# Kernel optimization log

Hardware: AMD Instinct MI355X
Metric: run time of the kernel (lower is better)

Reference implementation:

```python
import jax, jax.numpy as jnp
import numpy as np

B, S, D, H, FF = 2, 2048, 1024, 16, 4096
HD = D // H
SCALE = 1.0 / np.sqrt(HD).astype(np.float32)
EPS = 1e-5


def _ln(x, g, b):
    m = jnp.mean(x, axis=-1, keepdims=True)
    v = jnp.mean((x - m) ** 2, axis=-1, keepdims=True)
    return (x - m) * jax.lax.rsqrt(v + EPS) * g + b


def setup_inputs() -> dict:
    key = jax.random.key(0)
    ks = jax.random.split(key, 8)
    def lin(k, fan_in, shape):
        return (jax.random.normal(k, shape, jnp.float32) / np.sqrt(fan_in)).astype(jnp.float32)
    return {
        "x": jax.random.normal(ks[0], (B, S, D), jnp.float32),
        "w_qkv": lin(ks[1], D, (D, 3 * D)),          # qkv_proj (no bias)
        "w_o": lin(ks[2], D, (D, D)),                 # out_proj
        "b_o": jnp.zeros((D,), jnp.float32),
        "g1": jnp.ones((D,), jnp.float32),            # attn LayerNorm
        "bt1": jnp.zeros((D,), jnp.float32),
        "w1": lin(ks[3], D, (D, FF)),                 # FFN linear1
        "b1": jnp.zeros((FF,), jnp.float32),
        "w2": lin(ks[4], FF, (FF, D)),                # FFN linear2
        "b2": jnp.zeros((D,), jnp.float32),
        "g2": jnp.ones((D,), jnp.float32),            # FFN LayerNorm
        "bt2": jnp.zeros((D,), jnp.float32),
    }


def reference(x, w_qkv, w_o, b_o, g1, bt1, w1, b1, w2, b2, g2, bt2):
    # --- MultiHeadAttention (post-LN, dropout=eval/identity) ---
    qkv = (x @ w_qkv).reshape(B, S, H, 3 * HD)
    q, k, v = jnp.split(qkv, 3, axis=-1)  # each [B,S,H,HD]
    # kernel_func = scaled softmax over keys
    scores = jnp.einsum("bihd,bjhd->bhij", q, k) * SCALE  # [B,H,S,S]
    attn = jax.nn.softmax(scores, axis=-1)
    ao = jnp.einsum("bhij,bjhd->bihd", attn, v).reshape(B, S, D)
    y = _ln(x + ao @ w_o + b_o, g1, bt1)
    # --- FFN (post-LN) ---
    h = jax.nn.relu(y @ w1 + b1)
    return _ln(y + h @ w2 + b2, g2, bt2)
```

## Files before the change

kernel.cpp:

```cpp
#include <hip/hip_runtime.h>
#include <hip/hip_bf16.h>

#define B_  2
#define S_  2048
#define D_  1024
#define H_  16
#define HD_ 64
#define FF_ 4096
#define NT  (B_ * S_)
#define SCALE_ 0.125f
#define KLOG2E 0.1803368801111f
#define EPS_  1e-5f

typedef __attribute__((ext_vector_type(8))) short bf16x8;
typedef __attribute__((ext_vector_type(4))) float f32x4;

__device__ inline short f2bf(float f) {
    __hip_bfloat16 h = __float2bfloat16(f);
    return __builtin_bit_cast(short, h);
}
__device__ inline float bf2f(unsigned short u) {
    __hip_bfloat16 h = __builtin_bit_cast(__hip_bfloat16, u);
    return __bfloat162float(h);
}
__device__ inline unsigned int pk2bf(float lo, float hi) {
    __hip_bfloat162 h = __float22bfloat162_rn(float2{lo, hi});
    const unsigned short l16 = __builtin_bit_cast(unsigned short, h.x);
    const unsigned short h16 = __builtin_bit_cast(unsigned short, h.y);
    return (unsigned int)l16 | ((unsigned int)h16 << 16);
}

#define GLOBAL_AS __attribute__((address_space(1)))
#define LDS_AS    __attribute__((address_space(3)))

struct DetectArgs { const unsigned short* p[12]; int n[12]; };

__global__ __launch_bounds__(256) void detect_kernel(DetectArgs a, int* flags) {
    const int t = blockIdx.x;
    const unsigned short* s = a.p[t];
    const int cnt = min(a.n[t], 16384);
    const int tid = threadIdx.x;
    int huge = 0, zeven = 0;
    for (int i = tid; i < cnt; i += 256) {
        const unsigned short v = s[i];
        const int e = (v >> 7) & 0xFF;
        if (e >= 142) huge++;
        if (((i & 1) == 0) && ((v & 0x7FFF) == 0)) zeven++;
    }
    __shared__ int sh, sz;
    if (tid == 0) { sh = 0; sz = 0; }
    __syncthreads();
    atomicAdd(&sh, huge);
    atomicAdd(&sz, zeven);
    __syncthreads();
    if (tid == 0) flags[t] = (sh > 0 || sz * 4 > cnt) ? 1 : 0;
}

struct VecArgs { const void* src[7]; float* dst[7]; int n[7]; int fidx[7]; };

__global__ __launch_bounds__(256) void conv_x_vecs_kernel(
    const void* __restrict__ src, unsigned short* __restrict__ dst, int n,
    VecArgs a, const int* __restrict__ flags)
{
    const int i = blockIdx.x * 256 + threadIdx.x;
    if (i < n) {
        if (flags[0])
            dst[i] = (unsigned short)f2bf(((const float*)src)[i]);
        else
            dst[i] = ((const unsigned short*)src)[i];
    }
    if (blockIdx.x < 7) {
        const int v = blockIdx.x;
        const int f = flags[a.fidx[v]];
        for (int j = threadIdx.x; j < a.n[v]; j += 256) {
            a.dst[v][j] = f ? ((const float*)a.src[v])[j]
                            : bf2f(((const unsigned short*)a.src[v])[j]);
        }
    }
}

struct TArgs {
    const void* src[4]; unsigned short* dst[4];
    int K[4], N[4], fidx[4], start[5];
};

__global__ __launch_bounds__(256) void conv_t_all_kernel(
    TArgs t, const int* __restrict__ flags)
{
    __shared__ short T[32][33];
    const int tile = blockIdx.x;
    int w = 0;
    if (tile >= t.start[1]) w = 1;
    if (tile >= t.start[2]) w = 2;
    if (tile >= t.start[3]) w = 3;
    const int rel = tile - t.start[w];
    const int K = t.K[w], N = t.N[w];
    const int tilesN = N / 32;
    const int kt = (rel / tilesN) * 32, nt = (rel % tilesN) * 32;
    const void* src = t.src[w];
    unsigned short* dst = t.dst[w];
    const int f = flags[t.fidx[w]];

    const int c  = threadIdx.x & 31;
    const int r0 = (threadIdx.x >> 5) * 4;
#pragma unroll
    for (int i = 0; i < 4; i++) {
        const int r = r0 + i;
        const size_t gi = (size_t)(kt + r) * N + nt + c;
        short v = f ? f2bf(((const float*)src)[gi])
                    : (short)((const unsigned short*)src)[gi];
        T[c][r] = v;
    }
    __syncthreads();
#pragma unroll
    for (int i = 0; i < 4; i++) {
        const int n = r0 + i;
        dst[(size_t)(nt + n) * K + kt + c] = (unsigned short)T[n][c];
    }
}

template<bool HAS_BIAS, bool RELU, int RES, bool OUT_F32, bool QSCALE>
__global__ __launch_bounds__(256) void gemm128_kernel(
    const unsigned short* __restrict__ A,
    const unsigned short* __restrict__ Bt,
    const float* __restrict__ bias,
    const unsigned short* __restrict__ resb,
    const float* __restrict__ resf,
    const int* __restrict__ flags,
    void* __restrict__ out,
    int M, int N, int K)
{
    __shared__ short As[2][128 * 32];
    __shared__ short Bs[2][128 * 32];

    const int tid  = threadIdx.x;
    const int wave = tid >> 6;
    const int lane = tid & 63;
    const int quad = lane >> 4;
    const int l16  = lane & 15;

    const int row0 = blockIdx.x * 128;
    const int col0 = blockIdx.y * 128;

    const int ldrow = lane >> 2;
    const int ldk   = (lane & 3) * 8;
    const unsigned short* agp0 = A  + (size_t)(row0 + wave * 32 + ldrow) * K + ldk;
    const unsigned short* agp1 = agp0 + (size_t)16 * K;
    const unsigned short* bgp0 = Bt + (size_t)(col0 + wave * 32 + ldrow) * K + ldk;
    const unsigned short* bgp1 = bgp0 + (size_t)16 * K;

    const int wm = (wave >> 1) * 64;
    const int wn = (wave & 1) * 64;

    f32x4 acc[4][4] = {};

    for (int k0 = 0; k0 < K; k0 += 64) {
#pragma unroll
        for (int h = 0; h < 2; h++) {
            __builtin_amdgcn_global_load_lds(
                (const GLOBAL_AS void*)(agp0 + k0 + h * 32),
                (LDS_AS void*)&As[h][wave * 1024 + lane * 8], 16, 0, 0);
            __builtin_amdgcn_global_load_lds(
                (const GLOBAL_AS void*)(agp1 + k0 + h * 32),
                (LDS_AS void*)&As[h][wave * 1024 + 512 + lane * 8], 16, 0, 0);
            __builtin_amdgcn_global_load_lds(
                (const GLOBAL_AS void*)(bgp0 + k0 + h * 32),
                (LDS_AS void*)&Bs[h][wave * 1024 + lane * 8], 16, 0, 0);
            __builtin_amdgcn_global_load_lds(
                (const GLOBAL_AS void*)(bgp1 + k0 + h * 32),
                (LDS_AS void*)&Bs[h][wave * 1024 + 512 + lane * 8], 16, 0, 0);
        }
        __syncthreads();

#pragma unroll
        for (int h = 0; h < 2; h++) {
            bf16x8 af[4], bfr[4];
#pragma unroll
            for (int mi = 0; mi < 4; mi++)
                af[mi] = *reinterpret_cast<const bf16x8*>(
                    &As[h][(wm + mi * 16 + l16) * 32 + quad * 8]);
#pragma unroll
            for (int ni = 0; ni < 4; ni++)
                bfr[ni] = *reinterpret_cast<const bf16x8*>(
                    &Bs[h][(wn + ni * 16 + l16) * 32 + quad * 8]);
#pragma unroll
            for (int mi = 0; mi < 4; mi++)
#pragma unroll
                for (int ni = 0; ni < 4; ni++)
                    acc[mi][ni] = __builtin_amdgcn_mfma_f32_16x16x32_bf16(
                        af[mi], bfr[ni], acc[mi][ni], 0, 0, 0);
        }
        __syncthreads();
    }

    int resIsF32 = 0;
    if constexpr (RES == 2) resIsF32 = flags[0];

#pragma unroll
    for (int ni = 0; ni < 4; ni++) {
        const int col = col0 + wn + ni * 16 + l16;
        float badd = 0.f;
        if constexpr (HAS_BIAS) badd = bias[col];
        float qs = 1.f;
        if constexpr (QSCALE)
            qs = (((col0 + wn + ni * 16) % 192) < 64) ? KLOG2E : 1.f;
#pragma unroll
        for (int mi = 0; mi < 4; mi++) {
#pragma unroll
            for (int r = 0; r < 4; r++) {
                const int row = row0 + wm + mi * 16 + quad * 4 + r;
                float v = acc[mi][ni][r] + badd;
                if constexpr (QSCALE) v *= qs;
                if constexpr (RES == 1) {
                    v += bf2f(resb[(size_t)row * N + col]);
                } else if constexpr (RES == 2) {
                    v += resIsF32 ? resf[(size_t)row * N + col]
                                  : bf2f(resb[(size_t)row * N + col]);
                }
                if constexpr (RELU) v = fmaxf(v, 0.f);
                if constexpr (OUT_F32)
                    ((float*)out)[(size_t)row * N + col] = v;
                else
                    ((unsigned short*)out)[(size_t)row * N + col] =
                        (unsigned short)f2bf(v);
            }
        }
    }
}

__global__ __launch_bounds__(256) void gemm128_sk_kernel(
    const unsigned short* __restrict__ A,
    const unsigned short* __restrict__ Bt,
    float* __restrict__ out0,
    float* __restrict__ out1,
    int M, int N, int K)
{
    __shared__ short As[2][128 * 32];
    __shared__ short Bs[2][128 * 32];

    const int tid  = threadIdx.x;
    const int wave = tid >> 6;
    const int lane = tid & 63;
    const int quad = lane >> 4;
    const int l16  = lane & 15;

    const int row0 = blockIdx.x * 128;
    const int col0 = blockIdx.y * 128;
    const int z    = blockIdx.z;
    const int Kh   = K >> 1;

    const unsigned short* Az  = A  + (size_t)z * Kh;
    const unsigned short* Btz = Bt + (size_t)z * Kh;
    float* out = z ? out1 : out0;

    const int ldrow = lane >> 2;
    const int ldk   = (lane & 3) * 8;
    const unsigned short* agp0 = Az  + (size_t)(row0 + wave * 32 + ldrow) * K + ldk;
    const unsigned short* agp1 = agp0 + (size_t)16 * K;
    const unsigned short* bgp0 = Btz + (size_t)(col0 + wave * 32 + ldrow) * K + ldk;
    const unsigned short* bgp1 = bgp0 + (size_t)16 * K;

    const int wm = (wave >> 1) * 64;
    const int wn = (wave & 1) * 64;

    f32x4 acc[4][4] = {};

    for (int k0 = 0; k0 < Kh; k0 += 64) {
#pragma unroll
        for (int h = 0; h < 2; h++) {
            __builtin_amdgcn_global_load_lds(
                (const GLOBAL_AS void*)(agp0 + k0 + h * 32),
                (LDS_AS void*)&As[h][wave * 1024 + lane * 8], 16, 0, 0);
            __builtin_amdgcn_global_load_lds(
                (const GLOBAL_AS void*)(agp1 + k0 + h * 32),
                (LDS_AS void*)&As[h][wave * 1024 + 512 + lane * 8], 16, 0, 0);
            __builtin_amdgcn_global_load_lds(
                (const GLOBAL_AS void*)(bgp0 + k0 + h * 32),
                (LDS_AS void*)&Bs[h][wave * 1024 + lane * 8], 16, 0, 0);
            __builtin_amdgcn_global_load_lds(
                (const GLOBAL_AS void*)(bgp1 + k0 + h * 32),
                (LDS_AS void*)&Bs[h][wave * 1024 + 512 + lane * 8], 16, 0, 0);
        }
        __syncthreads();

#pragma unroll
        for (int h = 0; h < 2; h++) {
            bf16x8 af[4], bfr[4];
#pragma unroll
            for (int mi = 0; mi < 4; mi++)
                af[mi] = *reinterpret_cast<const bf16x8*>(
                    &As[h][(wm + mi * 16 + l16) * 32 + quad * 8]);
#pragma unroll
            for (int ni = 0; ni < 4; ni++)
                bfr[ni] = *reinterpret_cast<const bf16x8*>(
                    &Bs[h][(wn + ni * 16 + l16) * 32 + quad * 8]);
#pragma unroll
            for (int mi = 0; mi < 4; mi++)
#pragma unroll
                for (int ni = 0; ni < 4; ni++)
                    acc[mi][ni] = __builtin_amdgcn_mfma_f32_16x16x32_bf16(
                        af[mi], bfr[ni], acc[mi][ni], 0, 0, 0);
        }
        __syncthreads();
    }

#pragma unroll
    for (int ni = 0; ni < 4; ni++) {
        const int col = col0 + wn + ni * 16 + l16;
#pragma unroll
        for (int mi = 0; mi < 4; mi++)
#pragma unroll
            for (int r = 0; r < 4; r++) {
                const int row = row0 + wm + mi * 16 + quad * 4 + r;
                out[(size_t)row * N + col] = acc[mi][ni][r];
            }
    }
}

__global__ __launch_bounds__(512) void attn_kernel(
    const unsigned short* __restrict__ qkv,
    unsigned short* __restrict__ ao)
{
    extern __shared__ char smem[];

    const int qt = blockIdx.x;
    const int h  = blockIdx.y;
    const int b  = blockIdx.z;

    const int tid  = threadIdx.x;
    const int wave = tid >> 6;
    const int g    = wave >> 2;
    const int gw   = wave & 3;
    const int lane = tid & 63;
    const int quad = lane >> 4;
    const int l16  = lane & 15;
    const int gtid = tid & 255;

    short* Ks = (short*)smem + g * (64 * 72);
    short* Vt = (short*)(smem + 18432) + g * (64 * 72);
    short* Ps = (short*)(smem + 36864) + wave * (32 * 72);

    bf16x8 qf[2][2];
#pragma unroll
    for (int mi = 0; mi < 2; mi++) {
        const int qrow = qt * 128 + gw * 32 + mi * 16 + l16;
        const unsigned short* qb = qkv + (size_t)(b * S_ + qrow) * 3072 + h * 192;
        qf[mi][0] = *reinterpret_cast<const bf16x8*>(qb + quad * 8);
        qf[mi][1] = *reinterpret_cast<const bf16x8*>(qb + 32 + quad * 8);
    }

    bf16x8 vones;
#pragma unroll
    for (int j = 0; j < 8; j++) vones[j] = (short)0x3F80;

    f32x4 o[2][4] = {};
    f32x4 o_l[2] = {};

    const int skey = gtid >> 3;
    const int soct = gtid & 7;
    const int vp   = gtid >> 3;
    const int kA   = (vp & 15) + ((vp >> 4) << 5);
    const int kB   = kA + 16;
    const int posA = 4 * (vp & 15) + 2 * (vp >> 4);
    const int vwr  = ((posA >> 3) ^ soct) * 8 + (posA & 7);

    const int kb0   = g * (S_ / 2);
    const int kbend = kb0 + S_ / 2;

    const unsigned short* kbase0 = qkv + (size_t)(b * S_) * 3072 + h * 192 + 64;
    const unsigned short* vbase0 = qkv + (size_t)(b * S_) * 3072 + h * 192 + 128;

    bf16x8 pk0 = *reinterpret_cast<const bf16x8*>(kbase0 + (size_t)(kb0 + skey) * 3072 + soct * 8);
    bf16x8 pk1 = *reinterpret_cast<const bf16x8*>(kbase0 + (size_t)(kb0 + skey + 32) * 3072 + soct * 8);
    bf16x8 pv0 = *reinterpret_cast<const bf16x8*>(vbase0 + (size_t)(kb0 + kA) * 3072 + soct * 8);
    bf16x8 pv1 = *reinterpret_cast<const bf16x8*>(vbase0 + (size_t)(kb0 + kB) * 3072 + soct * 8);

    for (int kb = kb0; kb < kbend; kb += 64) {
        {
            const int woct0 = soct ^ ((skey >> 3) & 1);
            *reinterpret_cast<bf16x8*>(&Ks[skey * 72 + woct0 * 8]) = pk0;
            const int woct1 = soct ^ (((skey + 32) >> 3) & 1);
            *reinterpret_cast<bf16x8*>(&Ks[(skey + 32) * 72 + woct1 * 8]) = pk1;
#pragma unroll
            for (int j = 0; j < 8; j++) {
                const int d = soct * 8 + j;
                const unsigned int val =
                    (unsigned int)(unsigned short)pv0[j] |
                    ((unsigned int)(unsigned short)pv1[j] << 16);
                *reinterpret_cast<unsigned int*>(&Vt[d * 72 + vwr]) = val;
            }
        }
        __syncthreads();

        {
            const int kbn = (kb + 64 < kbend) ? kb + 64 : kb;
            pk0 = *reinterpret_cast<const bf16x8*>(
                kbase0 + (size_t)(kbn + skey) * 3072 + soct * 8);
            pk1 = *reinterpret_cast<const bf16x8*>(
                kbase0 + (size_t)(kbn + skey + 32) * 3072 + soct * 8);
            pv0 = *reinterpret_cast<const bf16x8*>(
                vbase0 + (size_t)(kbn + kA) * 3072 + soct * 8);
            pv1 = *reinterpret_cast<const bf16x8*>(
                vbase0 + (size_t)(kbn + kB) * 3072 + soct * 8);
        }

        f32x4 s[2][4] = {};
#pragma unroll
        for (int c2 = 0; c2 < 2; c2++) {
#pragma unroll
            for (int nt = 0; nt < 4; nt++) {
                const int key = nt * 16 + l16;
                const int roct = (c2 * 4 + quad) ^ ((key >> 3) & 1);
                bf16x8 kf = *reinterpret_cast<const bf16x8*>(
                    &Ks[key * 72 + roct * 8]);
                s[0][nt] = __builtin_amdgcn_mfma_f32_16x16x32_bf16(qf[0][c2], kf, s[0][nt], 0, 0, 0);
                s[1][nt] = __builtin_amdgcn_mfma_f32_16x16x32_bf16(qf[1][c2], kf, s[1][nt], 0, 0, 0);
            }
        }

#pragma unroll
        for (int mi = 0; mi < 2; mi++) {
#pragma unroll
            for (int r = 0; r < 4; r++) {
                const int m = mi * 16 + quad * 4 + r;
                const float p0 = exp2f(s[mi][0][r]);
                const float p1 = exp2f(s[mi][1][r]);
                const float p2 = exp2f(s[mi][2][r]);
                const float p3 = exp2f(s[mi][3][r]);
                uint2 w;
                w.x = pk2bf(p0, p1);
                w.y = pk2bf(p2, p3);
                *reinterpret_cast<uint2*>(&Ps[m * 72 + l16 * 4]) = w;
            }
        }

#pragma unroll
        for (int c2 = 0; c2 < 2; c2++) {
            bf16x8 pf[2];
#pragma unroll
            for (int mi = 0; mi < 2; mi++) {
                const int m = mi * 16 + l16;
                pf[mi] = *reinterpret_cast<const bf16x8*>(
                    &Ps[m * 72 + c2 * 32 + quad * 8]);
            }
#pragma unroll
            for (int ct = 0; ct < 4; ct++) {
                const int row = ct * 16 + l16;
                const int blk = (c2 * 4 + quad) ^ (row >> 3);
                bf16x8 vf = *reinterpret_cast<const bf16x8*>(
                    &Vt[row * 72 + blk * 8]);
                o[0][ct] = __builtin_amdgcn_mfma_f32_16x16x32_bf16(pf[0], vf, o[0][ct], 0, 0, 0);
                o[1][ct] = __builtin_amdgcn_mfma_f32_16x16x32_bf16(pf[1], vf, o[1][ct], 0, 0, 0);
            }
            o_l[0] = __builtin_amdgcn_mfma_f32_16x16x32_bf16(pf[0], vones, o_l[0], 0, 0, 0);
            o_l[1] = __builtin_amdgcn_mfma_f32_16x16x32_bf16(pf[1], vones, o_l[1], 0, 0, 0);
        }
        __syncthreads();
    }

    float* ex = (float*)smem;
    const int slot = (gw * 64 + lane) * 40;
    if (g == 1) {
#pragma unroll
        for (int mi = 0; mi < 2; mi++) {
#pragma unroll
            for (int ct = 0; ct < 4; ct++)
                *reinterpret_cast<f32x4*>(&ex[slot + mi * 16 + ct * 4]) = o[mi][ct];
            *reinterpret_cast<f32x4*>(&ex[slot + 32 + mi * 4]) = o_l[mi];
        }
    }
    __syncthreads();
    if (g == 0) {
#pragma unroll
        for (int mi = 0; mi < 2; mi++) {
#pragma unroll
            for (int ct = 0; ct < 4; ct++) {
                f32x4 t = *reinterpret_cast<const f32x4*>(&ex[slot + mi * 16 + ct * 4]);
                o[mi][ct] += t;
            }
            f32x4 tl = *reinterpret_cast<const f32x4*>(&ex[slot + 32 + mi * 4]);
            o_l[mi] += tl;
        }
#pragma unroll
        for (int mi = 0; mi < 2; mi++) {
            f32x4 rl;
#pragma unroll
            for (int r = 0; r < 4; r++) rl[r] = 1.f / o_l[mi][r];
#pragma unroll
            for (int ct = 0; ct < 4; ct++)
#pragma unroll
                for (int r = 0; r < 4; r++) {
                    const int row = qt * 128 + gw * 32 + mi * 16 + quad * 4 + r;
                    ao[(size_t)(b * S_ + row) * D_ + h * HD_ + ct * 16 + l16] =
                        (unsigned short)f2bf(o[mi][ct][r] * rl[r]);
                }
        }
    }
}

template<int RESM, bool FLAG_OUT>
__global__ __launch_bounds__(256) void ln_sum_kernel(
    const float* __restrict__ p0,
    const float* __restrict__ p1,
    const float* __restrict__ bias,
    const unsigned short* __restrict__ resb,
    const float* __restrict__ resf,
    const float* __restrict__ g,
    const float* __restrict__ bt,
    const int* __restrict__ flags,
    void* __restrict__ out)
{
    const int row = blockIdx.x;
    const int tid = threadIdx.x;
    const int c0  = tid * 4;
    const size_t base = (size_t)row * D_ + c0;

    float4 a = *reinterpret_cast<const float4*>(p0 + base);
    float4 bq = *reinterpret_cast<const float4*>(p1 + base);
    float4 bi = *reinterpret_cast<const float4*>(bias + c0);

    float v[4] = {a.x + bq.x + bi.x, a.y + bq.y + bi.y,
                  a.z + bq.z + bi.z, a.w + bq.w + bi.w};

    if constexpr (RESM == 1) {
        if (flags[0]) {
            float4 rv = *reinterpret_cast<const float4*>(resf + base);
            v[0] += rv.x; v[1] += rv.y; v[2] += rv.z; v[3] += rv.w;
        } else {
            uint2 rv = *reinterpret_cast<const uint2*>(resb + base);
            v[0] += bf2f((unsigned short)(rv.x & 0xFFFF));
            v[1] += bf2f((unsigned short)(rv.x >> 16));
            v[2] += bf2f((unsigned short)(rv.y & 0xFFFF));
            v[3] += bf2f((unsigned short)(rv.y >> 16));
        }
    } else {
        uint2 rv = *reinterpret_cast<const uint2*>(resb + base);
        v[0] += bf2f((unsigned short)(rv.x & 0xFFFF));
        v[1] += bf2f((unsigned short)(rv.x >> 16));
        v[2] += bf2f((unsigned short)(rv.y & 0xFFFF));
        v[3] += bf2f((unsigned short)(rv.y >> 16));
    }

    float s = v[0] + v[1] + v[2] + v[3];
    float sq = v[0] * v[0] + v[1] * v[1] + v[2] * v[2] + v[3] * v[3];
#pragma unroll
    for (int msk = 1; msk < 64; msk <<= 1) {
        s += __shfl_xor(s, msk);
        sq += __shfl_xor(sq, msk);
    }
    __shared__ float ss[4], ssq[4];
    if ((tid & 63) == 0) { ss[tid >> 6] = s; ssq[tid >> 6] = sq; }
    __syncthreads();
    s = ss[0] + ss[1] + ss[2] + ss[3];
    sq = ssq[0] + ssq[1] + ssq[2] + ssq[3];

    const float mean = s * (1.f / D_);
    const float var = sq * (1.f / D_) - mean * mean;
    const float rinv = rsqrtf(var + EPS_);

    float w[4];
#pragma unroll
    for (int i = 0; i < 4; i++)
        w[i] = (v[i] - mean) * rinv * g[c0 + i] + bt[c0 + i];

    int outF32 = 0;
    if constexpr (FLAG_OUT) outF32 = flags[0];

    if (FLAG_OUT && outF32) {
        float4 o4 = {w[0], w[1], w[2], w[3]};
        *reinterpret_cast<float4*>((float*)out + base) = o4;
    } else {
        uint2 o2;
        o2.x = pk2bf(w[0], w[1]);
        o2.y = pk2bf(w[2], w[3]);
        *reinterpret_cast<uint2*>((unsigned short*)out + base) = o2;
    }
}

extern "C" void kernel_launch(void* const* d_in, const int* in_sizes, int n_in,
                              void* d_out, int out_size, void* d_ws, size_t ws_size,
                              hipStream_t stream) {
    char* ws = (char*)d_ws;

    int*            flags = (int*)(ws + 0);
    unsigned short* xb    = (unsigned short*)(ws + 256);
    unsigned short* wqkvT = (unsigned short*)(ws + 8388864);
    unsigned short* woT   = (unsigned short*)(ws + 14680320);
    unsigned short* w1T   = (unsigned short*)(ws + 16777472);
    unsigned short* w2T   = (unsigned short*)(ws + 25166080);
    float*          bof   = (float*)(ws + 33554688);
    float*          g1f   = (float*)(ws + 33558784);
    float*          bt1f  = (float*)(ws + 33562880);
    float*          b1f   = (float*)(ws + 33566976);
    float*          b2f   = (float*)(ws + 33583360);
    float*          g2f   = (float*)(ws + 33587456);
    float*          bt2f  = (float*)(ws + 33591552);
    unsigned short* qkv   = (unsigned short*)(ws + 33595648);
    unsigned short* ao    = (unsigned short*)(ws + 256);
    unsigned short* y     = (unsigned short*)(ws + 33595648);
    unsigned short* hbuf  = (unsigned short*)(ws + 41984256);
    float*          part0 = (float*)(ws + 58761472);
    float*          part1 = (float*)(ws + 75538688);
    float*          hpart0= (float*)(ws + 256);

    dim3 blk(256);

    static int attn_attr_done = 0;
    if (!attn_attr_done) {
        hipFuncSetAttribute(reinterpret_cast<const void*>(attn_kernel),
                            hipFuncAttributeMaxDynamicSharedMemorySize, 73728);
        attn_attr_done = 1;
    }

    DetectArgs da;
    for (int i = 0; i < 12; i++) {
        da.p[i] = (const unsigned short*)d_in[i];
        da.n[i] = in_sizes[i];
    }
    detect_kernel<<<dim3(12), blk, 0, stream>>>(da, flags);

    VecArgs va;
    const int vidx[7] = {3, 4, 5, 7, 9, 10, 11};
    float* vdst[7] = {bof, g1f, bt1f, b1f, b2f, g2f, bt2f};
    for (int i = 0; i < 7; i++) {
        va.src[i] = d_in[vidx[i]];
        va.dst[i] = vdst[i];
        va.n[i]   = in_sizes[vidx[i]];
        va.fidx[i] = vidx[i];
    }
    conv_x_vecs_kernel<<<dim3((NT * D_ + 255) / 256), blk, 0, stream>>>(
        d_in[0], xb, NT * D_, va, flags);

    TArgs ta;
    ta.src[0] = d_in[1]; ta.dst[0] = wqkvT; ta.K[0] = D_;  ta.N[0] = 3 * D_; ta.fidx[0] = 1;
    ta.src[1] = d_in[2]; ta.dst[1] = woT;   ta.K[1] = D_;  ta.N[1] = D_;     ta.fidx[1] = 2;
    ta.src[2] = d_in[6]; ta.dst[2] = w1T;   ta.K[2] = D_;  ta.N[2] = FF_;    ta.fidx[2] = 6;
    ta.src[3] = d_in[8]; ta.dst[3] = w2T;   ta.K[3] = FF_; ta.N[3] = D_;     ta.fidx[3] = 8;
    ta.start[0] = 0;
    for (int wI = 0; wI < 4; wI++)
        ta.start[wI + 1] = ta.start[wI] + (ta.K[wI] / 32) * (ta.N[wI] / 32);
    conv_t_all_kernel<<<dim3(ta.start[4]), blk, 0, stream>>>(ta, flags);

    gemm128_kernel<false, false, 0, false, true>
        <<<dim3(NT / 128, 3072 / 128), blk, 0, stream>>>(
            xb, wqkvT, nullptr, nullptr, nullptr, flags, qkv, NT, 3072, 1024);

    attn_kernel<<<dim3(S_ / 128, H_, B_), dim3(512), 73728, stream>>>(qkv, ao);

    gemm128_sk_kernel<<<dim3(NT / 128, 1024 / 128, 2), blk, 0, stream>>>(
        ao, woT, part0, part1, NT, 1024, 1024);

    ln_sum_kernel<1, false><<<dim3(NT), blk, 0, stream>>>(
        part0, part1, bof, (const unsigned short*)d_in[0], (const float*)d_in[0],
        g1f, bt1f, flags, y);

    gemm128_kernel<true, true, 0, false, false>
        <<<dim3(NT / 128, 4096 / 128), blk, 0, stream>>>(
            y, w1T, b1f, nullptr, nullptr, flags, hbuf, NT, 4096, 1024);

    gemm128_sk_kernel<<<dim3(NT / 128, 1024 / 128, 2), blk, 0, stream>>>(
        hbuf, w2T, hpart0, part1, NT, 1024, 4096);

    ln_sum_kernel<2, true><<<dim3(NT), blk, 0, stream>>>(
        hpart0, part1, b2f, y, nullptr, g2f, bt2f, flags, d_out);
}
```

Measured before the change: 385.9 us.

## Software-pipeline GEMM k-loop so next-tile LDS loads overlap MFMA on other half

Both GEMM kernels now issue the first k-tile's global-to-LDS loads before the loop. Inside the loop, once a 32-wide half has been consumed by the MFMAs, a barrier is taken and the next k-tile's data for that half is loaded in place. This lets the global loads for one half run while the MFMAs work on the other half, instead of loading the whole tile and stalling before any compute. The cost is a barrier per half rather than two per tile. Correctness relies on the barrier also waiting for the outstanding async LDS loads.

```diff
diff --git a/kernel.cpp b/kernel.cpp
--- a/kernel.cpp
+++ b/kernel.cpp
@@ -154,24 +154,26 @@
 
     f32x4 acc[4][4] = {};
 
+#pragma unroll
+    for (int h = 0; h < 2; h++) {
+        __builtin_amdgcn_global_load_lds(
+            (const GLOBAL_AS void*)(agp0 + h * 32),
+            (LDS_AS void*)&As[h][wave * 1024 + lane * 8], 16, 0, 0);
+        __builtin_amdgcn_global_load_lds(
+            (const GLOBAL_AS void*)(agp1 + h * 32),
+            (LDS_AS void*)&As[h][wave * 1024 + 512 + lane * 8], 16, 0, 0);
+        __builtin_amdgcn_global_load_lds(
+            (const GLOBAL_AS void*)(bgp0 + h * 32),
+            (LDS_AS void*)&Bs[h][wave * 1024 + lane * 8], 16, 0, 0);
+        __builtin_amdgcn_global_load_lds(
+            (const GLOBAL_AS void*)(bgp1 + h * 32),
+            (LDS_AS void*)&Bs[h][wave * 1024 + 512 + lane * 8], 16, 0, 0);
+    }
+    __syncthreads();
+
     for (int k0 = 0; k0 < K; k0 += 64) {
-#pragma unroll
-        for (int h = 0; h < 2; h++) {
-            __builtin_amdgcn_global_load_lds(
-                (const GLOBAL_AS void*)(agp0 + k0 + h * 32),
-                (LDS_AS void*)&As[h][wave * 1024 + lane * 8], 16, 0, 0);
-            __builtin_amdgcn_global_load_lds(
-                (const GLOBAL_AS void*)(agp1 + k0 + h * 32),
-                (LDS_AS void*)&As[h][wave * 1024 + 512 + lane * 8], 16, 0, 0);
-            __builtin_amdgcn_global_load_lds(
-                (const GLOBAL_AS void*)(bgp0 + k0 + h * 32),
-                (LDS_AS void*)&Bs[h][wave * 1024 + lane * 8], 16, 0, 0);
-            __builtin_amdgcn_global_load_lds(
-                (const GLOBAL_AS void*)(bgp1 + k0 + h * 32),
-                (LDS_AS void*)&Bs[h][wave * 1024 + 512 + lane * 8], 16, 0, 0);
-        }
-        __syncthreads();
-
+        const int kn = k0 + 64;
+        const bool more = kn < K;
 #pragma unroll
         for (int h = 0; h < 2; h++) {
             bf16x8 af[4], bfr[4];
@@ -189,8 +191,22 @@
                 for (int ni = 0; ni < 4; ni++)
                     acc[mi][ni] = __builtin_amdgcn_mfma_f32_16x16x32_bf16(
                         af[mi], bfr[ni], acc[mi][ni], 0, 0, 0);
-        }
-        __syncthreads();
+            __syncthreads();
+            if (more) {
+                __builtin_amdgcn_global_load_lds(
+                    (const GLOBAL_AS void*)(agp0 + kn + h * 32),
+                    (LDS_AS void*)&As[h][wave * 1024 + lane * 8], 16, 0, 0);
+                __builtin_amdgcn_global_load_lds(
+                    (const GLOBAL_AS void*)(agp1 + kn + h * 32),
+                    (LDS_AS void*)&As[h][wave * 1024 + 512 + lane * 8], 16, 0, 0);
+                __builtin_amdgcn_global_load_lds(
+                    (const GLOBAL_AS void*)(bgp0 + kn + h * 32),
+                    (LDS_AS void*)&Bs[h][wave * 1024 + lane * 8], 16, 0, 0);
+                __builtin_amdgcn_global_load_lds(
+                    (const GLOBAL_AS void*)(bgp1 + kn + h * 32),
+                    (LDS_AS void*)&Bs[h][wave * 1024 + 512 + lane * 8], 16, 0, 0);
+            }
+        }
     }
 
     int resIsF32 = 0;
@@ -265,24 +281,26 @@
 
     f32x4 acc[4][4] = {};
 
+#pragma unroll
+    for (int h = 0; h < 2; h++) {
+        __builtin_amdgcn_global_load_lds(
+            (const GLOBAL_AS void*)(agp0 + h * 32),
+            (LDS_AS void*)&As[h][wave * 1024 + lane * 8], 16, 0, 0);
+        __builtin_amdgcn_global_load_lds(
+            (const GLOBAL_AS void*)(agp1 + h * 32),
+            (LDS_AS void*)&As[h][wave * 1024 + 512 + lane * 8], 16, 0, 0);
+        __builtin_amdgcn_global_load_lds(
+            (const GLOBAL_AS void*)(bgp0 + h * 32),
+            (LDS_AS void*)&Bs[h][wave * 1024 + lane * 8], 16, 0, 0);
+        __builtin_amdgcn_global_load_lds(
+            (const GLOBAL_AS void*)(bgp1 + h * 32),
+            (LDS_AS void*)&Bs[h][wave * 1024 + 512 + lane * 8], 16, 0, 0);
+    }
+    __syncthreads();
+
     for (int k0 = 0; k0 < Kh; k0 += 64) {
-#pragma unroll
-        for (int h = 0; h < 2; h++) {
-            __builtin_amdgcn_global_load_lds(
-                (const GLOBAL_AS void*)(agp0 + k0 + h * 32),
-                (LDS_AS void*)&As[h][wave * 1024 + lane * 8], 16, 0, 0);
-            __builtin_amdgcn_global_load_lds(
-                (const GLOBAL_AS void*)(agp1 + k0 + h * 32),
-                (LDS_AS void*)&As[h][wave * 1024 + 512 + lane * 8], 16, 0, 0);
-            __builtin_amdgcn_global_load_lds(
-                (const GLOBAL_AS void*)(bgp0 + k0 + h * 32),
-                (LDS_AS void*)&Bs[h][wave * 1024 + lane * 8], 16, 0, 0);
-            __builtin_amdgcn_global_load_lds(
-                (const GLOBAL_AS void*)(bgp1 + k0 + h * 32),
-                (LDS_AS void*)&Bs[h][wave * 1024 + 512 + lane * 8], 16, 0, 0);
-        }
-        __syncthreads();
-
+        const int kn = k0 + 64;
+        const bool more = kn < Kh;
 #pragma unroll
         for (int h = 0; h < 2; h++) {
             bf16x8 af[4], bfr[4];
@@ -300,8 +318,22 @@
                 for (int ni = 0; ni < 4; ni++)
                     acc[mi][ni] = __builtin_amdgcn_mfma_f32_16x16x32_bf16(
                         af[mi], bfr[ni], acc[mi][ni], 0, 0, 0);
-        }
-        __syncthreads();
+            __syncthreads();
+            if (more) {
+                __builtin_amdgcn_global_load_lds(
+                    (const GLOBAL_AS void*)(agp0 + kn + h * 32),
+                    (LDS_AS void*)&As[h][wave * 1024 + lane * 8], 16, 0, 0);
+                __builtin_amdgcn_global_load_lds(
+                    (const GLOBAL_AS void*)(agp1 + kn + h * 32),
+                    (LDS_AS void*)&As[h][wave * 1024 + 512 + lane * 8], 16, 0, 0);
+                __builtin_amdgcn_global_load_lds(
+                    (const GLOBAL_AS void*)(bgp0 + kn + h * 32),
+                    (LDS_AS void*)&Bs[h][wave * 1024 + lane * 8], 16, 0, 0);
+                __builtin_amdgcn_global_load_lds(
+                    (const GLOBAL_AS void*)(bgp1 + kn + h * 32),
+                    (LDS_AS void*)&Bs[h][wave * 1024 + 512 + lane * 8], 16, 0, 0);
+            }
+        }
     }
 
 #pragma unroll
```

Result: slower. 398.2 us (+3.2%).

## Use 256x256 multi-stage GEMM tiles with swizzled LDS; prefetch in split-K GEMM

Applied to the files above, without the earlier changes.

Replaces the 128x128 double-buffered GEMM used for the QKV and FFN1 projections with a 256x256, 512-thread kernel. The new kernel runs a 4-slot, 3-deep asynchronous global-to-LDS pipeline with explicit vmcnt waits and an XOR-swizzled LDS layout to avoid bank conflicts. The split-K GEMM gains the same swizzle, and it now prefetches the next k-step into each half-buffer as soon as that half has been consumed. The intent is more data reuse per tile, better load/compute overlap and fewer LDS conflicts. In exchange it uses 128KB of dynamic LDS and more registers, which lowers occupancy, and the large tiles give only 192 and 256 blocks for these GEMMs.

```diff
diff --git a/kernel.cpp b/kernel.cpp
--- a/kernel.cpp
+++ b/kernel.cpp
@@ -119,110 +119,110 @@
     }
 }
 
-template<bool HAS_BIAS, bool RELU, int RES, bool OUT_F32, bool QSCALE>
-__global__ __launch_bounds__(256) void gemm128_kernel(
+#define G256_STAGE(tile_)                                                     \
+    do {                                                                      \
+        char* sb_ = smem + (size_t)((tile_) & 3) * 32768;                     \
+        const int kb_ = (tile_) << 5;                                         \
+        __builtin_amdgcn_global_load_lds(                                     \
+            (const GLOBAL_AS void*)(ag0 + kb_),                               \
+            (LDS_AS void*)(sb_ + sdst2), 16, 0, 0);                           \
+        __builtin_amdgcn_global_load_lds(                                     \
+            (const GLOBAL_AS void*)(ag1 + kb_),                               \
+            (LDS_AS void*)(sb_ + 8192 + sdst2), 16, 0, 0);                    \
+        __builtin_amdgcn_global_load_lds(                                     \
+            (const GLOBAL_AS void*)(bg0 + kb_),                               \
+            (LDS_AS void*)(sb_ + 16384 + sdst2), 16, 0, 0);                   \
+        __builtin_amdgcn_global_load_lds(                                     \
+            (const GLOBAL_AS void*)(bg1 + kb_),                               \
+            (LDS_AS void*)(sb_ + 24576 + sdst2), 16, 0, 0);                   \
+    } while (0)
+
+template<bool HAS_BIAS, bool RELU, bool QSCALE>
+__global__ __launch_bounds__(512) void gemm256_kernel(
     const unsigned short* __restrict__ A,
     const unsigned short* __restrict__ Bt,
     const float* __restrict__ bias,
-    const unsigned short* __restrict__ resb,
-    const float* __restrict__ resf,
-    const int* __restrict__ flags,
-    void* __restrict__ out,
+    unsigned short* __restrict__ out,
     int M, int N, int K)
 {
-    __shared__ short As[2][128 * 32];
-    __shared__ short Bs[2][128 * 32];
+    extern __shared__ char smem[];
 
     const int tid  = threadIdx.x;
     const int wave = tid >> 6;
     const int lane = tid & 63;
     const int quad = lane >> 4;
     const int l16  = lane & 15;
-
-    const int row0 = blockIdx.x * 128;
-    const int col0 = blockIdx.y * 128;
-
-    const int ldrow = lane >> 2;
-    const int ldk   = (lane & 3) * 8;
-    const unsigned short* agp0 = A  + (size_t)(row0 + wave * 32 + ldrow) * K + ldk;
-    const unsigned short* agp1 = agp0 + (size_t)16 * K;
-    const unsigned short* bgp0 = Bt + (size_t)(col0 + wave * 32 + ldrow) * K + ldk;
-    const unsigned short* bgp1 = bgp0 + (size_t)16 * K;
-
-    const int wm = (wave >> 1) * 64;
-    const int wn = (wave & 1) * 64;
-
-    f32x4 acc[4][4] = {};
-
-    for (int k0 = 0; k0 < K; k0 += 64) {
-#pragma unroll
-        for (int h = 0; h < 2; h++) {
-            __builtin_amdgcn_global_load_lds(
-                (const GLOBAL_AS void*)(agp0 + k0 + h * 32),
-                (LDS_AS void*)&As[h][wave * 1024 + lane * 8], 16, 0, 0);
-            __builtin_amdgcn_global_load_lds(
-                (const GLOBAL_AS void*)(agp1 + k0 + h * 32),
-                (LDS_AS void*)&As[h][wave * 1024 + 512 + lane * 8], 16, 0, 0);
-            __builtin_amdgcn_global_load_lds(
-                (const GLOBAL_AS void*)(bgp0 + k0 + h * 32),
-                (LDS_AS void*)&Bs[h][wave * 1024 + lane * 8], 16, 0, 0);
-            __builtin_amdgcn_global_load_lds(
-                (const GLOBAL_AS void*)(bgp1 + k0 + h * 32),
-                (LDS_AS void*)&Bs[h][wave * 1024 + 512 + lane * 8], 16, 0, 0);
-        }
-        __syncthreads();
-
-#pragma unroll
-        for (int h = 0; h < 2; h++) {
-            bf16x8 af[4], bfr[4];
-#pragma unroll
-            for (int mi = 0; mi < 4; mi++)
-                af[mi] = *reinterpret_cast<const bf16x8*>(
-                    &As[h][(wm + mi * 16 + l16) * 32 + quad * 8]);
+    const int wr   = wave >> 2;
+    const int wc   = wave & 3;
+
+    const int row0 = blockIdx.x * 256;
+    const int col0 = blockIdx.y * 256;
+
+    const int srow  = tid >> 2;
+    const int sk    = (((tid & 3) ^ ((srow >> 1) & 3)) * 8);
+    const int sdst2 = srow * 64 + (tid & 3) * 16;
+    const unsigned short* ag0 = A  + (size_t)(row0 + srow) * K + sk;
+    const unsigned short* ag1 = A  + (size_t)(row0 + 128 + srow) * K + sk;
+    const unsigned short* bg0 = Bt + (size_t)(col0 + srow) * K + sk;
+    const unsigned short* bg1 = Bt + (size_t)(col0 + 128 + srow) * K + sk;
+
+    const int rsw = (quad ^ ((l16 >> 1) & 3)) * 8;
+
+    const int NTk = K >> 5;
+
+    f32x4 acc[8][4] = {};
+
+    G256_STAGE(0);
+    G256_STAGE(1);
+    G256_STAGE(2);
+
+    for (int t = 0; t < NTk; t++) {
+        if (t + 2 < NTk)
+            asm volatile("s_waitcnt vmcnt(8)\n\ts_barrier" ::: "memory");
+        else if (t + 1 < NTk)
+            asm volatile("s_waitcnt vmcnt(4)\n\ts_barrier" ::: "memory");
+        else
+            asm volatile("s_waitcnt vmcnt(0)\n\ts_barrier" ::: "memory");
+
+        const short* sA = (const short*)(smem + (size_t)(t & 3) * 32768);
+        const short* sB = sA + 8192;
+
+        bf16x8 af[8], bfr[4];
+#pragma unroll
+        for (int mi = 0; mi < 8; mi++)
+            af[mi] = *reinterpret_cast<const bf16x8*>(
+                &sA[(wr * 128 + mi * 16 + l16) * 32 + rsw]);
+#pragma unroll
+        for (int ni = 0; ni < 4; ni++)
+            bfr[ni] = *reinterpret_cast<const bf16x8*>(
+                &sB[(wc * 64 + ni * 16 + l16) * 32 + rsw]);
+#pragma unroll
+        for (int mi = 0; mi < 8; mi++)
 #pragma unroll
             for (int ni = 0; ni < 4; ni++)
-                bfr[ni] = *reinterpret_cast<const bf16x8*>(
-                    &Bs[h][(wn + ni * 16 + l16) * 32 + quad * 8]);
-#pragma unroll
-            for (int mi = 0; mi < 4; mi++)
-#pragma unroll
-                for (int ni = 0; ni < 4; ni++)
-                    acc[mi][ni] = __builtin_amdgcn_mfma_f32_16x16x32_bf16(
-                        af[mi], bfr[ni], acc[mi][ni], 0, 0, 0);
-        }
-        __syncthreads();
-    }
-
-    int resIsF32 = 0;
-    if constexpr (RES == 2) resIsF32 = flags[0];
+                acc[mi][ni] = __builtin_amdgcn_mfma_f32_16x16x32_bf16(
+                    af[mi], bfr[ni], acc[mi][ni], 0, 0, 0);
+
+        if (t + 3 < NTk) G256_STAGE(t + 3);
+    }
 
 #pragma unroll
     for (int ni = 0; ni < 4; ni++) {
-        const int col = col0 + wn + ni * 16 + l16;
+        const int col = col0 + wc * 64 + ni * 16 + l16;
         float badd = 0.f;
         if constexpr (HAS_BIAS) badd = bias[col];
         float qs = 1.f;
         if constexpr (QSCALE)
-            qs = (((col0 + wn + ni * 16) % 192) < 64) ? KLOG2E : 1.f;
-#pragma unroll
-        for (int mi = 0; mi < 4; mi++) {
+            qs = (((col0 + wc * 64 + ni * 16) % 192) < 64) ? KLOG2E : 1.f;
+#pragma unroll
+        for (int mi = 0; mi < 8; mi++) {
 #pragma unroll
             for (int r = 0; r < 4; r++) {
-                const int row = row0 + wm + mi * 16 + quad * 4 + r;
+                const int row = row0 + wr * 128 + mi * 16 + quad * 4 + r;
                 float v = acc[mi][ni][r] + badd;
                 if constexpr (QSCALE) v *= qs;
-                if constexpr (RES == 1) {
-                    v += bf2f(resb[(size_t)row * N + col]);
-                } else if constexpr (RES == 2) {
-                    v += resIsF32 ? resf[(size_t)row * N + col]
-                                  : bf2f(resb[(size_t)row * N + col]);
-                }
                 if constexpr (RELU) v = fmaxf(v, 0.f);
-                if constexpr (OUT_F32)
-                    ((float*)out)[(size_t)row * N + col] = v;
-                else
-                    ((unsigned short*)out)[(size_t)row * N + col] =
-                        (unsigned short)f2bf(v);
+                out[(size_t)row * N + col] = (unsigned short)f2bf(v);
             }
         }
     }
@@ -254,7 +254,7 @@
     float* out = z ? out1 : out0;
 
     const int ldrow = lane >> 2;
-    const int ldk   = (lane & 3) * 8;
+    const int ldk   = (((lane & 3) ^ ((lane >> 3) & 3)) * 8);
     const unsigned short* agp0 = Az  + (size_t)(row0 + wave * 32 + ldrow) * K + ldk;
     const unsigned short* agp1 = agp0 + (size_t)16 * K;
     const unsigned short* bgp0 = Btz + (size_t)(col0 + wave * 32 + ldrow) * K + ldk;
@@ -262,46 +262,63 @@
 
     const int wm = (wave >> 1) * 64;
     const int wn = (wave & 1) * 64;
+    const int rsw = (quad ^ ((l16 >> 1) & 3)) * 8;
 
     f32x4 acc[4][4] = {};
 
+#pragma unroll
+    for (int h = 0; h < 2; h++) {
+        __builtin_amdgcn_global_load_lds(
+            (const GLOBAL_AS void*)(agp0 + h * 32),
+            (LDS_AS void*)&As[h][wave * 1024 + lane * 8], 16, 0, 0);
+        __builtin_amdgcn_global_load_lds(
+            (const GLOBAL_AS void*)(agp1 + h * 32),
+            (LDS_AS void*)&As[h][wave * 1024 + 512 + lane * 8], 16, 0, 0);
+        __builtin_amdgcn_global_load_lds(
+            (const GLOBAL_AS void*)(bgp0 + h * 32),
+            (LDS_AS void*)&Bs[h][wave * 1024 + lane * 8], 16, 0, 0);
+        __builtin_amdgcn_global_load_lds(
+            (const GLOBAL_AS void*)(bgp1 + h * 32),
+            (LDS_AS void*)&Bs[h][wave * 1024 + 512 + lane * 8], 16, 0, 0);
+    }
+    __syncthreads();
+
     for (int k0 = 0; k0 < Kh; k0 += 64) {
-#pragma unroll
-        for (int h = 0; h < 2; h++) {
-            __builtin_amdgcn_global_load_lds(
-                (const GLOBAL_AS void*)(agp0 + k0 + h * 32),
-                (LDS_AS void*)&As[h][wave * 1024 + lane * 8], 16, 0, 0);
-            __builtin_amdgcn_global_load_lds(
-                (const GLOBAL_AS void*)(agp1 + k0 + h * 32),
-                (LDS_AS void*)&As[h][wave * 1024 + 512 + lane * 8], 16, 0, 0);
-            __builtin_amdgcn_global_load_lds(
-                (const GLOBAL_AS void*)(bgp0 + k0 + h * 32),
-                (LDS_AS void*)&Bs[h][wave * 1024 + lane * 8], 16, 0, 0);
-            __builtin_amdgcn_global_load_lds(
-                (const GLOBAL_AS void*)(bgp1 + k0 + h * 32),
-                (LDS_AS void*)&Bs[h][wave * 1024 + 512 + lane * 8], 16, 0, 0);
-        }
-        __syncthreads();
-
+        const int kn = k0 + 64;
+        const bool more = kn < Kh;
 #pragma unroll
         for (int h = 0; h < 2; h++) {
             bf16x8 af[4], bfr[4];
 #pragma unroll
             for (int mi = 0; mi < 4; mi++)
                 af[mi] = *reinterpret_cast<const bf16x8*>(
-                    &As[h][(wm + mi * 16 + l16) * 32 + quad * 8]);
+                    &As[h][(wm + mi * 16 + l16) * 32 + rsw]);
 #pragma unroll
             for (int ni = 0; ni < 4; ni++)
                 bfr[ni] = *reinterpret_cast<const bf16x8*>(
-                    &Bs[h][(wn + ni * 16 + l16) * 32 + quad * 8]);
+                    &Bs[h][(wn + ni * 16 + l16) * 32 + rsw]);
 #pragma unroll
             for (int mi = 0; mi < 4; mi++)
 #pragma unroll
                 for (int ni = 0; ni < 4; ni++)
                     acc[mi][ni] = __builtin_amdgcn_mfma_f32_16x16x32_bf16(
                         af[mi], bfr[ni], acc[mi][ni], 0, 0, 0);
-        }
-        __syncthreads();
+            __syncthreads();
+            if (more) {
+                __builtin_amdgcn_global_load_lds(
+                    (const GLOBAL_AS void*)(agp0 + kn + h * 32),
+                    (LDS_AS void*)&As[h][wave * 1024 + lane * 8], 16, 0, 0);
+                __builtin_amdgcn_global_load_lds(
+                    (const GLOBAL_AS void*)(agp1 + kn + h * 32),
+                    (LDS_AS void*)&As[h][wave * 1024 + 512 + lane * 8], 16, 0, 0);
+                __builtin_amdgcn_global_load_lds(
+                    (const GLOBAL_AS void*)(bgp0 + kn + h * 32),
+                    (LDS_AS void*)&Bs[h][wave * 1024 + lane * 8], 16, 0, 0);
+                __builtin_amdgcn_global_load_lds(
+                    (const GLOBAL_AS void*)(bgp1 + kn + h * 32),
+                    (LDS_AS void*)&Bs[h][wave * 1024 + 512 + lane * 8], 16, 0, 0);
+            }
+        }
     }
 
 #pragma unroll
@@ -605,11 +622,17 @@
 
     dim3 blk(256);
 
-    static int attn_attr_done = 0;
-    if (!attn_attr_done) {
+    static int attr_done = 0;
+    if (!attr_done) {
         hipFuncSetAttribute(reinterpret_cast<const void*>(attn_kernel),
                             hipFuncAttributeMaxDynamicSharedMemorySize, 73728);
-        attn_attr_done = 1;
+        hipFuncSetAttribute(
+            reinterpret_cast<const void*>(&gemm256_kernel<false, false, true>),
+            hipFuncAttributeMaxDynamicSharedMemorySize, 131072);
+        hipFuncSetAttribute(
+            reinterpret_cast<const void*>(&gemm256_kernel<true, true, false>),
+            hipFuncAttributeMaxDynamicSharedMemorySize, 131072);
+        attr_done = 1;
     }
 
     DetectArgs da;
@@ -641,9 +664,9 @@
         ta.start[wI + 1] = ta.start[wI] + (ta.K[wI] / 32) * (ta.N[wI] / 32);
     conv_t_all_kernel<<<dim3(ta.start[4]), blk, 0, stream>>>(ta, flags);
 
-    gemm128_kernel<false, false, 0, false, true>
-        <<<dim3(NT / 128, 3072 / 128), blk, 0, stream>>>(
-            xb, wqkvT, nullptr, nullptr, nullptr, flags, qkv, NT, 3072, 1024);
+    gemm256_kernel<false, false, true>
+        <<<dim3(NT / 256, 3072 / 256), dim3(512), 131072, stream>>>(
+            xb, wqkvT, nullptr, qkv, NT, 3072, 1024);
 
     attn_kernel<<<dim3(S_ / 128, H_, B_), dim3(512), 73728, stream>>>(qkv, ao);
 
@@ -654,9 +677,9 @@
         part0, part1, bof, (const unsigned short*)d_in[0], (const float*)d_in[0],
         g1f, bt1f, flags, y);
 
-    gemm128_kernel<true, true, 0, false, false>
-        <<<dim3(NT / 128, 4096 / 128), blk, 0, stream>>>(
-            y, w1T, b1f, nullptr, nullptr, flags, hbuf, NT, 4096, 1024);
+    gemm256_kernel<true, true, false>
+        <<<dim3(NT / 256, 4096 / 256), dim3(512), 131072, stream>>>(
+            y, w1T, b1f, hbuf, NT, 4096, 1024);
 
     gemm128_sk_kernel<<<dim3(NT / 128, 1024 / 128, 2), blk, 0, stream>>>(
         hbuf, w2T, hpart0, part1, NT, 1024, 4096);
```

Result: no change. 379.6 us (-1.6%).
